# Performance work log

Measured on AMD Instinct MI355X. Metric: run time of the kernel, lower is better.

## Reference

```python
import jax, jax.numpy as jnp
import numpy as np

B = 65536
D = 8          # model dim (hard-wired in source)
H = 2          # num_heads
A = 20         # act_size
L = 5          # tokens per embedding stream


def _attn_layer(x, Wqkv, bqkv, Wo, bo, Wl, bl):
    # x: [B, S, D]
    Bx, S, Dx = x.shape
    hd = Dx // H
    qkv = x @ Wqkv.T + bqkv                      # [B, S, 3D]
    q, k, v = jnp.split(qkv, 3, axis=-1)
    def split_heads(t):
        return t.reshape(Bx, S, H, hd).transpose(0, 2, 1, 3)  # [B,H,S,hd]
    q, k, v = split_heads(q), split_heads(k), split_heads(v)
    scores = jnp.einsum('bhqd,bhkd->bhqk', q, k) * (hd ** -0.5)
    attn = jax.nn.softmax(scores, axis=-1)       # dropout inactive at eval
    o = jnp.einsum('bhqk,bhkd->bhqd', attn, v)
    o = o.transpose(0, 2, 1, 3).reshape(Bx, S, Dx)
    x = x + (o @ Wo.T + bo)                      # residual after attention
    h = jax.nn.relu(x @ Wl.T + bl)               # linear + relu
    return x + h                                 # second residual


def setup_inputs() -> dict:
    key = jax.random.key(0)
    ks = jax.random.split(key, 20)
    s = 1.0 / np.sqrt(D)
    inp = {
        'dice_type': jax.random.randint(ks[0], (B, L), 0, 15),
        'dice_star': jax.random.randint(ks[1], (B, L), 0, 15),
        'summon_lvl': jax.random.randint(ks[2], (B, L), 0, 2),
        'emb_dice': jax.random.normal(ks[3], (15, D), jnp.float32),
        'emb_star': jax.random.normal(ks[4], (15, D), jnp.float32),
        'emb_btns': jax.random.normal(ks[5], (2, D), jnp.float32),
        'Wout': jax.random.normal(ks[6], (A, D), jnp.float32) * s,
        'bout': jnp.zeros((A,), jnp.float32),
    }
    for i in range(2):
        o = 7 + 5 * i
        inp[f'Wqkv{i}'] = jax.random.normal(ks[o], (3 * D, D), jnp.float32) * s
        inp[f'bqkv{i}'] = jnp.zeros((3 * D,), jnp.float32)
        inp[f'Wo{i}'] = jax.random.normal(ks[o + 1], (D, D), jnp.float32) * s
        inp[f'bo{i}'] = jnp.zeros((D,), jnp.float32)
        inp[f'Wl{i}'] = jax.random.normal(ks[o + 2], (D, D), jnp.float32) * s
        inp[f'bl{i}'] = jnp.zeros((D,), jnp.float32)
    return inp


def reference(dice_type, dice_star, summon_lvl,
              emb_dice, emb_star, emb_btns,
              Wqkv0, bqkv0, Wo0, bo0, Wl0, bl0,
              Wqkv1, bqkv1, Wo1, bo1, Wl1, bl1,
              Wout, bout):
    x = jnp.concatenate([emb_dice[dice_type],
                         emb_star[dice_star],
                         emb_btns[summon_lvl]], axis=1)  # [B, 15, D]
    x = _attn_layer(x, Wqkv0, bqkv0, Wo0, bo0, Wl0, bl0)
    x = _attn_layer(x, Wqkv1, bqkv1, Wo1, bo1, Wl1, bl1)
    x = jnp.mean(x, axis=1)                               # [B, D]
    return x @ Wout.T + bout                              # [B, A]
```

## Files before the change

kernel.cpp:

```cpp
#include <hip/hip_runtime.h>
#include <math.h>

#define EPB 16
#define BTOT 65536

__device__ __forceinline__ float fast_exp2(float x) {
#if defined(__has_builtin)
#if __has_builtin(__builtin_amdgcn_exp2f)
  return __builtin_amdgcn_exp2f(x);
#else
  return exp2f(x);
#endif
#else
  return exp2f(x);
#endif
}

__device__ __forceinline__ void attn_layer(
    float x[8], int e, int t,
    const float* __restrict__ Wqkv, const float* __restrict__ bqkv,
    const float* __restrict__ Wo, const float* __restrict__ bo,
    const float* __restrict__ Wl, const float* __restrict__ bl,
    float (*kb)[17][8], float (*vb)[17][8])
{
  float q[8];
  if (t < 15) {
    float k[8], v[8];
#pragma unroll
    for (int c = 0; c < 8; ++c) {
      float aq = bqkv[c];
      float ak = bqkv[8 + c];
      float av = bqkv[16 + c];
#pragma unroll
      for (int j = 0; j < 8; ++j) {
        aq = fmaf(x[j], Wqkv[c * 8 + j], aq);
        ak = fmaf(x[j], Wqkv[(8 + c) * 8 + j], ak);
        av = fmaf(x[j], Wqkv[(16 + c) * 8 + j], av);
      }
      q[c] = aq; k[c] = ak; v[c] = av;
    }
    float4* kd = (float4*)kb[e][t];
    kd[0] = make_float4(k[0], k[1], k[2], k[3]);
    kd[1] = make_float4(k[4], k[5], k[6], k[7]);
    float4* vd = (float4*)vb[e][t];
    vd[0] = make_float4(v[0], v[1], v[2], v[3]);
    vd[1] = make_float4(v[4], v[5], v[6], v[7]);
  }
  __syncthreads();
  if (t < 15) {
    float s0[15], s1[15];
#pragma unroll
    for (int u = 0; u < 15; ++u) {
      const float4 k0 = *(const float4*)(kb[e][u]);
      const float4 k1 = *(const float4*)(kb[e][u] + 4);
      float a0 = q[0] * k0.x;
      a0 = fmaf(q[1], k0.y, a0); a0 = fmaf(q[2], k0.z, a0); a0 = fmaf(q[3], k0.w, a0);
      float a1 = q[4] * k1.x;
      a1 = fmaf(q[5], k1.y, a1); a1 = fmaf(q[6], k1.z, a1); a1 = fmaf(q[7], k1.w, a1);
      s0[u] = a0 * 0.5f;
      s1[u] = a1 * 0.5f;
    }
    float m0 = s0[0], m1 = s1[0];
#pragma unroll
    for (int u = 1; u < 15; ++u) { m0 = fmaxf(m0, s0[u]); m1 = fmaxf(m1, s1[u]); }
    float sum0 = 0.f, sum1 = 0.f;
#pragma unroll
    for (int u = 0; u < 15; ++u) {
      s0[u] = fast_exp2((s0[u] - m0) * 1.4426950408889634f);
      s1[u] = fast_exp2((s1[u] - m1) * 1.4426950408889634f);
      sum0 += s0[u]; sum1 += s1[u];
    }
    const float r0 = 1.0f / sum0, r1 = 1.0f / sum1;
    float o[8] = {0.f, 0.f, 0.f, 0.f, 0.f, 0.f, 0.f, 0.f};
#pragma unroll
    for (int u = 0; u < 15; ++u) {
      const float4 v0 = *(const float4*)(vb[e][u]);
      const float4 v1 = *(const float4*)(vb[e][u] + 4);
      o[0] = fmaf(s0[u], v0.x, o[0]); o[1] = fmaf(s0[u], v0.y, o[1]);
      o[2] = fmaf(s0[u], v0.z, o[2]); o[3] = fmaf(s0[u], v0.w, o[3]);
      o[4] = fmaf(s1[u], v1.x, o[4]); o[5] = fmaf(s1[u], v1.y, o[5]);
      o[6] = fmaf(s1[u], v1.z, o[6]); o[7] = fmaf(s1[u], v1.w, o[7]);
    }
#pragma unroll
    for (int d = 0; d < 4; ++d) { o[d] *= r0; o[4 + d] *= r1; }
    float xn[8];
#pragma unroll
    for (int c = 0; c < 8; ++c) {
      float acc = bo[c];
#pragma unroll
      for (int j = 0; j < 8; ++j) acc = fmaf(o[j], Wo[c * 8 + j], acc);
      xn[c] = x[c] + acc;
    }
#pragma unroll
    for (int c = 0; c < 8; ++c) {
      float acc = bl[c];
#pragma unroll
      for (int j = 0; j < 8; ++j) acc = fmaf(xn[j], Wl[c * 8 + j], acc);
      x[c] = xn[c] + fmaxf(acc, 0.0f);
    }
  }
  __syncthreads();
}

__global__ __launch_bounds__(256) void BetterBot_44169443672375_kernel(
    const int* __restrict__ dice_type, const int* __restrict__ dice_star,
    const int* __restrict__ summon_lvl,
    const float* __restrict__ emb_dice, const float* __restrict__ emb_star,
    const float* __restrict__ emb_btns,
    const float* __restrict__ Wout, const float* __restrict__ bout,
    const float* __restrict__ Wqkv0, const float* __restrict__ bqkv0,
    const float* __restrict__ Wo0, const float* __restrict__ bo0,
    const float* __restrict__ Wl0, const float* __restrict__ bl0,
    const float* __restrict__ Wqkv1, const float* __restrict__ bqkv1,
    const float* __restrict__ Wo1, const float* __restrict__ bo1,
    const float* __restrict__ Wl1, const float* __restrict__ bl1,
    float* __restrict__ out)
{
  __shared__ __align__(16) float kb[EPB][17][8];
  __shared__ __align__(16) float vb[EPB][17][8];
  const int tid = threadIdx.x;
  const int e = tid >> 4;
  const int t = tid & 15;
  const int ge = blockIdx.x * EPB + e;

  float x[8];
  if (t < 15) {
    const float* row;
    if (t < 5)       row = emb_dice + 8 * dice_type[ge * 5 + t];
    else if (t < 10) row = emb_star + 8 * dice_star[ge * 5 + (t - 5)];
    else             row = emb_btns + 8 * summon_lvl[ge * 5 + (t - 10)];
    const float4 r0 = *(const float4*)row;
    const float4 r1 = *(const float4*)(row + 4);
    x[0] = r0.x; x[1] = r0.y; x[2] = r0.z; x[3] = r0.w;
    x[4] = r1.x; x[5] = r1.y; x[6] = r1.z; x[7] = r1.w;
  }

  attn_layer(x, e, t, Wqkv0, bqkv0, Wo0, bo0, Wl0, bl0, kb, vb);
  attn_layer(x, e, t, Wqkv1, bqkv1, Wo1, bo1, Wl1, bl1, kb, vb);

  if (t < 15) {
    float4* xd = (float4*)kb[e][t];
    xd[0] = make_float4(x[0], x[1], x[2], x[3]);
    xd[1] = make_float4(x[4], x[5], x[6], x[7]);
  }
  __syncthreads();
  if (t < 8) {
    float s = 0.f;
#pragma unroll
    for (int u = 0; u < 15; ++u) s += kb[e][u][t];
    vb[e][0][t] = s * (1.0f / 15.0f);
  }
  __syncthreads();
  const int obase = blockIdx.x * (EPB * 20);
  for (int idx = tid; idx < EPB * 20; idx += 256) {
    const int e2 = idx / 20;
    const int a = idx - e2 * 20;
    const float* mr = vb[e2][0];
    float acc = bout[a];
#pragma unroll
    for (int j = 0; j < 8; ++j) acc = fmaf(mr[j], Wout[a * 8 + j], acc);
    out[obase + idx] = acc;
  }
}

extern "C" void kernel_launch(void* const* d_in, const int* in_sizes, int n_in,
                              void* d_out, int out_size, void* d_ws, size_t ws_size,
                              hipStream_t stream) {
  const int*   dice_type  = (const int*)d_in[0];
  const int*   dice_star  = (const int*)d_in[1];
  const int*   summon_lvl = (const int*)d_in[2];
  const float* emb_dice   = (const float*)d_in[3];
  const float* emb_star   = (const float*)d_in[4];
  const float* emb_btns   = (const float*)d_in[5];
  const float* Wout       = (const float*)d_in[6];
  const float* bout       = (const float*)d_in[7];
  const float* Wqkv0      = (const float*)d_in[8];
  const float* bqkv0      = (const float*)d_in[9];
  const float* Wo0        = (const float*)d_in[10];
  const float* bo0        = (const float*)d_in[11];
  const float* Wl0        = (const float*)d_in[12];
  const float* bl0        = (const float*)d_in[13];
  const float* Wqkv1      = (const float*)d_in[14];
  const float* bqkv1      = (const float*)d_in[15];
  const float* Wo1        = (const float*)d_in[16];
  const float* bo1        = (const float*)d_in[17];
  const float* Wl1        = (const float*)d_in[18];
  const float* bl1        = (const float*)d_in[19];
  float* out = (float*)d_out;

  dim3 grid(BTOT / EPB), block(256);
  hipLaunchKernelGGL(BetterBot_44169443672375_kernel, grid, block, 0, stream,
                     dice_type, dice_star, summon_lvl,
                     emb_dice, emb_star, emb_btns, Wout, bout,
                     Wqkv0, bqkv0, Wo0, bo0, Wl0, bl0,
                     Wqkv1, bqkv1, Wo1, bo1, Wl1, bl1,
                     out);
}
```

Measured before the change: 138.8 us.

## Map two tokens per thread, fuse softmax without max, shuffle-reduce mean

Each thread now processes two tokens, so 8 lanes cover one 15-token element and a block handles 32 elements. The separate max, exp and sum passes are fused into a single loop over keys, with the softmax scale and log2(e) folded into q. The max subtraction is dropped. The sequence mean is computed with cross-lane shuffles instead of shared memory and two extra barriers, and each lane writes part of its element's output row directly. This reduces barriers and the passes over K/V in LDS, and spreads the projection and attention work over more lanes. In exchange, register pressure per thread roughly doubles, and skipping the max subtraction risks exp overflow if scores grow large.

```diff
diff --git a/kernel.cpp b/kernel.cpp
--- a/kernel.cpp
+++ b/kernel.cpp
@@ -1,10 +1,12 @@
 #include <hip/hip_runtime.h>
 #include <math.h>
 
-#define EPB 16
+#define EPB 32
+#define ESTRIDE 132
 #define BTOT 65536
-
-__device__ __forceinline__ float fast_exp2(float x) {
+#define C_SCALE 0.72134752044f
+
+__device__ __forceinline__ float exp2_fast(float x) {
 #if defined(__has_builtin)
 #if __has_builtin(__builtin_amdgcn_exp2f)
   return __builtin_amdgcn_exp2f(x);
@@ -17,14 +19,15 @@
 }
 
 __device__ __forceinline__ void attn_layer(
-    float x[8], int e, int t,
+    float x[2][8], float* kb, float* vb, int g,
     const float* __restrict__ Wqkv, const float* __restrict__ bqkv,
     const float* __restrict__ Wo, const float* __restrict__ bo,
-    const float* __restrict__ Wl, const float* __restrict__ bl,
-    float (*kb)[17][8], float (*vb)[17][8])
+    const float* __restrict__ Wl, const float* __restrict__ bl)
 {
-  float q[8];
-  if (t < 15) {
+  float q[2][8];
+#pragma unroll
+  for (int i = 0; i < 2; ++i) {
+    const int t = 2 * g + i;
     float k[8], v[8];
 #pragma unroll
     for (int c = 0; c < 8; ++c) {
@@ -33,70 +36,65 @@
       float av = bqkv[16 + c];
 #pragma unroll
       for (int j = 0; j < 8; ++j) {
-        aq = fmaf(x[j], Wqkv[c * 8 + j], aq);
-        ak = fmaf(x[j], Wqkv[(8 + c) * 8 + j], ak);
-        av = fmaf(x[j], Wqkv[(16 + c) * 8 + j], av);
+        aq = fmaf(x[i][j], Wqkv[c * 8 + j], aq);
+        ak = fmaf(x[i][j], Wqkv[(8 + c) * 8 + j], ak);
+        av = fmaf(x[i][j], Wqkv[(16 + c) * 8 + j], av);
       }
-      q[c] = aq; k[c] = ak; v[c] = av;
-    }
-    float4* kd = (float4*)kb[e][t];
+      q[i][c] = aq * C_SCALE;
+      k[c] = ak; v[c] = av;
+    }
+    float4* kd = (float4*)(kb + t * 8);
     kd[0] = make_float4(k[0], k[1], k[2], k[3]);
     kd[1] = make_float4(k[4], k[5], k[6], k[7]);
-    float4* vd = (float4*)vb[e][t];
+    float4* vd = (float4*)(vb + t * 8);
     vd[0] = make_float4(v[0], v[1], v[2], v[3]);
     vd[1] = make_float4(v[4], v[5], v[6], v[7]);
   }
   __syncthreads();
-  if (t < 15) {
-    float s0[15], s1[15];
-#pragma unroll
-    for (int u = 0; u < 15; ++u) {
-      const float4 k0 = *(const float4*)(kb[e][u]);
-      const float4 k1 = *(const float4*)(kb[e][u] + 4);
-      float a0 = q[0] * k0.x;
-      a0 = fmaf(q[1], k0.y, a0); a0 = fmaf(q[2], k0.z, a0); a0 = fmaf(q[3], k0.w, a0);
-      float a1 = q[4] * k1.x;
-      a1 = fmaf(q[5], k1.y, a1); a1 = fmaf(q[6], k1.z, a1); a1 = fmaf(q[7], k1.w, a1);
-      s0[u] = a0 * 0.5f;
-      s1[u] = a1 * 0.5f;
-    }
-    float m0 = s0[0], m1 = s1[0];
-#pragma unroll
-    for (int u = 1; u < 15; ++u) { m0 = fmaxf(m0, s0[u]); m1 = fmaxf(m1, s1[u]); }
-    float sum0 = 0.f, sum1 = 0.f;
-#pragma unroll
-    for (int u = 0; u < 15; ++u) {
-      s0[u] = fast_exp2((s0[u] - m0) * 1.4426950408889634f);
-      s1[u] = fast_exp2((s1[u] - m1) * 1.4426950408889634f);
-      sum0 += s0[u]; sum1 += s1[u];
-    }
-    const float r0 = 1.0f / sum0, r1 = 1.0f / sum1;
-    float o[8] = {0.f, 0.f, 0.f, 0.f, 0.f, 0.f, 0.f, 0.f};
-#pragma unroll
-    for (int u = 0; u < 15; ++u) {
-      const float4 v0 = *(const float4*)(vb[e][u]);
-      const float4 v1 = *(const float4*)(vb[e][u] + 4);
-      o[0] = fmaf(s0[u], v0.x, o[0]); o[1] = fmaf(s0[u], v0.y, o[1]);
-      o[2] = fmaf(s0[u], v0.z, o[2]); o[3] = fmaf(s0[u], v0.w, o[3]);
-      o[4] = fmaf(s1[u], v1.x, o[4]); o[5] = fmaf(s1[u], v1.y, o[5]);
-      o[6] = fmaf(s1[u], v1.z, o[6]); o[7] = fmaf(s1[u], v1.w, o[7]);
-    }
-#pragma unroll
-    for (int d = 0; d < 4; ++d) { o[d] *= r0; o[4 + d] *= r1; }
+  float o[2][8] = {{0.f,0.f,0.f,0.f,0.f,0.f,0.f,0.f},
+                   {0.f,0.f,0.f,0.f,0.f,0.f,0.f,0.f}};
+  float sum00 = 0.f, sum01 = 0.f, sum10 = 0.f, sum11 = 0.f;
+#pragma unroll
+  for (int u = 0; u < 15; ++u) {
+    const float4 k0 = *(const float4*)(kb + u * 8);
+    const float4 k1 = *(const float4*)(kb + u * 8 + 4);
+    const float4 v0 = *(const float4*)(vb + u * 8);
+    const float4 v1 = *(const float4*)(vb + u * 8 + 4);
+#pragma unroll
+    for (int i = 0; i < 2; ++i) {
+      float s0 = q[i][0] * k0.x;
+      s0 = fmaf(q[i][1], k0.y, s0); s0 = fmaf(q[i][2], k0.z, s0); s0 = fmaf(q[i][3], k0.w, s0);
+      float s1 = q[i][4] * k1.x;
+      s1 = fmaf(q[i][5], k1.y, s1); s1 = fmaf(q[i][6], k1.z, s1); s1 = fmaf(q[i][7], k1.w, s1);
+      const float e0 = exp2_fast(s0);
+      const float e1 = exp2_fast(s1);
+      if (i == 0) { sum00 += e0; sum01 += e1; } else { sum10 += e0; sum11 += e1; }
+      o[i][0] = fmaf(e0, v0.x, o[i][0]); o[i][1] = fmaf(e0, v0.y, o[i][1]);
+      o[i][2] = fmaf(e0, v0.z, o[i][2]); o[i][3] = fmaf(e0, v0.w, o[i][3]);
+      o[i][4] = fmaf(e1, v1.x, o[i][4]); o[i][5] = fmaf(e1, v1.y, o[i][5]);
+      o[i][6] = fmaf(e1, v1.z, o[i][6]); o[i][7] = fmaf(e1, v1.w, o[i][7]);
+    }
+  }
+#pragma unroll
+  for (int i = 0; i < 2; ++i) {
+    const float r0 = 1.0f / (i == 0 ? sum00 : sum10);
+    const float r1 = 1.0f / (i == 0 ? sum01 : sum11);
+#pragma unroll
+    for (int d = 0; d < 4; ++d) { o[i][d] *= r0; o[i][4 + d] *= r1; }
     float xn[8];
 #pragma unroll
     for (int c = 0; c < 8; ++c) {
       float acc = bo[c];
 #pragma unroll
-      for (int j = 0; j < 8; ++j) acc = fmaf(o[j], Wo[c * 8 + j], acc);
-      xn[c] = x[c] + acc;
+      for (int j = 0; j < 8; ++j) acc = fmaf(o[i][j], Wo[c * 8 + j], acc);
+      xn[c] = x[i][c] + acc;
     }
 #pragma unroll
     for (int c = 0; c < 8; ++c) {
       float acc = bl[c];
 #pragma unroll
       for (int j = 0; j < 8; ++j) acc = fmaf(xn[j], Wl[c * 8 + j], acc);
-      x[c] = xn[c] + fmaxf(acc, 0.0f);
+      x[i][c] = xn[c] + fmaxf(acc, 0.0f);
     }
   }
   __syncthreads();
@@ -116,50 +114,61 @@
     const float* __restrict__ Wl1, const float* __restrict__ bl1,
     float* __restrict__ out)
 {
-  __shared__ __align__(16) float kb[EPB][17][8];
-  __shared__ __align__(16) float vb[EPB][17][8];
+  __shared__ __align__(16) float kb_s[EPB * ESTRIDE];
+  __shared__ __align__(16) float vb_s[EPB * ESTRIDE];
   const int tid = threadIdx.x;
-  const int e = tid >> 4;
-  const int t = tid & 15;
+  const int e = tid >> 3;
+  const int g = tid & 7;
   const int ge = blockIdx.x * EPB + e;
-
-  float x[8];
-  if (t < 15) {
-    const float* row;
-    if (t < 5)       row = emb_dice + 8 * dice_type[ge * 5 + t];
-    else if (t < 10) row = emb_star + 8 * dice_star[ge * 5 + (t - 5)];
-    else             row = emb_btns + 8 * summon_lvl[ge * 5 + (t - 10)];
-    const float4 r0 = *(const float4*)row;
-    const float4 r1 = *(const float4*)(row + 4);
-    x[0] = r0.x; x[1] = r0.y; x[2] = r0.z; x[3] = r0.w;
-    x[4] = r1.x; x[5] = r1.y; x[6] = r1.z; x[7] = r1.w;
-  }
-
-  attn_layer(x, e, t, Wqkv0, bqkv0, Wo0, bo0, Wl0, bl0, kb, vb);
-  attn_layer(x, e, t, Wqkv1, bqkv1, Wo1, bo1, Wl1, bl1, kb, vb);
-
-  if (t < 15) {
-    float4* xd = (float4*)kb[e][t];
-    xd[0] = make_float4(x[0], x[1], x[2], x[3]);
-    xd[1] = make_float4(x[4], x[5], x[6], x[7]);
-  }
-  __syncthreads();
-  if (t < 8) {
-    float s = 0.f;
-#pragma unroll
-    for (int u = 0; u < 15; ++u) s += kb[e][u][t];
-    vb[e][0][t] = s * (1.0f / 15.0f);
-  }
-  __syncthreads();
-  const int obase = blockIdx.x * (EPB * 20);
-  for (int idx = tid; idx < EPB * 20; idx += 256) {
-    const int e2 = idx / 20;
-    const int a = idx - e2 * 20;
-    const float* mr = vb[e2][0];
-    float acc = bout[a];
-#pragma unroll
-    for (int j = 0; j < 8; ++j) acc = fmaf(mr[j], Wout[a * 8 + j], acc);
-    out[obase + idx] = acc;
+  float* kb = kb_s + e * ESTRIDE;
+  float* vb = vb_s + e * ESTRIDE;
+
+  float x[2][8];
+#pragma unroll
+  for (int i = 0; i < 2; ++i) {
+    const int t = 2 * g + i;
+    if (t < 15) {
+      const float* row;
+      if (t < 5)       row = emb_dice + 8 * dice_type[ge * 5 + t];
+      else if (t < 10) row = emb_star + 8 * dice_star[ge * 5 + (t - 5)];
+      else             row = emb_btns + 8 * summon_lvl[ge * 5 + (t - 10)];
+      const float4 r0 = ((const float4*)row)[0];
+      const float4 r1 = ((const float4*)row)[1];
+      x[i][0] = r0.x; x[i][1] = r0.y; x[i][2] = r0.z; x[i][3] = r0.w;
+      x[i][4] = r1.x; x[i][5] = r1.y; x[i][6] = r1.z; x[i][7] = r1.w;
+    } else {
+#pragma unroll
+      for (int j = 0; j < 8; ++j) x[i][j] = 0.f;
+    }
+  }
+
+  attn_layer(x, kb, vb, g, Wqkv0, bqkv0, Wo0, bo0, Wl0, bl0);
+  attn_layer(x, kb, vb, g, Wqkv1, bqkv1, Wo1, bo1, Wl1, bl1);
+
+  const bool pad = (g == 7);
+  float p[8];
+#pragma unroll
+  for (int j = 0; j < 8; ++j) p[j] = x[0][j] + (pad ? 0.f : x[1][j]);
+#pragma unroll
+  for (int j = 0; j < 8; ++j) p[j] += __shfl_xor(p[j], 1);
+#pragma unroll
+  for (int j = 0; j < 8; ++j) p[j] += __shfl_xor(p[j], 2);
+#pragma unroll
+  for (int j = 0; j < 8; ++j) p[j] += __shfl_xor(p[j], 4);
+  float mean[8];
+#pragma unroll
+  for (int j = 0; j < 8; ++j) mean[j] = p[j] * (1.0f / 15.0f);
+
+  const int obase = ge * 20;
+#pragma unroll
+  for (int r = 0; r < 3; ++r) {
+    const int a = r * 8 + g;
+    if (a < 20) {
+      float acc = bout[a];
+#pragma unroll
+      for (int j = 0; j < 8; ++j) acc = fmaf(mean[j], Wout[a * 8 + j], acc);
+      out[obase + a] = acc;
+    }
   }
 }
 
```

After: 179.1 us. +29.0%, slower.

## Precompute layer-0 QKV and attention exps over the 32-token vocabulary table

Applied to the files above, without the earlier changes.

Layer 0 depends only on the token index, so each block computes QKV for all 32 possible embedding rows and the full 32x32 table of unnormalised exp scores once. Each token then gathers from these shared tables instead of doing its own projection and dot products. Layer 1 drops the max subtraction and fuses the exp into the PV loop, with the softmax scale folded into q. The mean reduction now uses wave shuffles and the output projection is computed directly per element, which removes two barriers. Omitting the max subtraction risks overflow if scores grow large, and every block redundantly rebuilds the table.

```diff
diff --git a/kernel.cpp b/kernel.cpp
--- a/kernel.cpp
+++ b/kernel.cpp
@@ -3,8 +3,10 @@
 
 #define EPB 16
 #define BTOT 65536
-
-__device__ __forceinline__ float fast_exp2(float x) {
+#define C_SCALE 0.72134752044f
+#define QSTR 28
+
+__device__ __forceinline__ float exp2_fast(float x) {
 #if defined(__has_builtin)
 #if __has_builtin(__builtin_amdgcn_exp2f)
   return __builtin_amdgcn_exp2f(x);
@@ -14,92 +16,6 @@
 #else
   return exp2f(x);
 #endif
-}
-
-__device__ __forceinline__ void attn_layer(
-    float x[8], int e, int t,
-    const float* __restrict__ Wqkv, const float* __restrict__ bqkv,
-    const float* __restrict__ Wo, const float* __restrict__ bo,
-    const float* __restrict__ Wl, const float* __restrict__ bl,
-    float (*kb)[17][8], float (*vb)[17][8])
-{
-  float q[8];
-  if (t < 15) {
-    float k[8], v[8];
-#pragma unroll
-    for (int c = 0; c < 8; ++c) {
-      float aq = bqkv[c];
-      float ak = bqkv[8 + c];
-      float av = bqkv[16 + c];
-#pragma unroll
-      for (int j = 0; j < 8; ++j) {
-        aq = fmaf(x[j], Wqkv[c * 8 + j], aq);
-        ak = fmaf(x[j], Wqkv[(8 + c) * 8 + j], ak);
-        av = fmaf(x[j], Wqkv[(16 + c) * 8 + j], av);
-      }
-      q[c] = aq; k[c] = ak; v[c] = av;
-    }
-    float4* kd = (float4*)kb[e][t];
-    kd[0] = make_float4(k[0], k[1], k[2], k[3]);
-    kd[1] = make_float4(k[4], k[5], k[6], k[7]);
-    float4* vd = (float4*)vb[e][t];
-    vd[0] = make_float4(v[0], v[1], v[2], v[3]);
-    vd[1] = make_float4(v[4], v[5], v[6], v[7]);
-  }
-  __syncthreads();
-  if (t < 15) {
-    float s0[15], s1[15];
-#pragma unroll
-    for (int u = 0; u < 15; ++u) {
-      const float4 k0 = *(const float4*)(kb[e][u]);
-      const float4 k1 = *(const float4*)(kb[e][u] + 4);
-      float a0 = q[0] * k0.x;
-      a0 = fmaf(q[1], k0.y, a0); a0 = fmaf(q[2], k0.z, a0); a0 = fmaf(q[3], k0.w, a0);
-      float a1 = q[4] * k1.x;
-      a1 = fmaf(q[5], k1.y, a1); a1 = fmaf(q[6], k1.z, a1); a1 = fmaf(q[7], k1.w, a1);
-      s0[u] = a0 * 0.5f;
-      s1[u] = a1 * 0.5f;
-    }
-    float m0 = s0[0], m1 = s1[0];
-#pragma unroll
-    for (int u = 1; u < 15; ++u) { m0 = fmaxf(m0, s0[u]); m1 = fmaxf(m1, s1[u]); }
-    float sum0 = 0.f, sum1 = 0.f;
-#pragma unroll
-    for (int u = 0; u < 15; ++u) {
-      s0[u] = fast_exp2((s0[u] - m0) * 1.4426950408889634f);
-      s1[u] = fast_exp2((s1[u] - m1) * 1.4426950408889634f);
-      sum0 += s0[u]; sum1 += s1[u];
-    }
-    const float r0 = 1.0f / sum0, r1 = 1.0f / sum1;
-    float o[8] = {0.f, 0.f, 0.f, 0.f, 0.f, 0.f, 0.f, 0.f};
-#pragma unroll
-    for (int u = 0; u < 15; ++u) {
-      const float4 v0 = *(const float4*)(vb[e][u]);
-      const float4 v1 = *(const float4*)(vb[e][u] + 4);
-      o[0] = fmaf(s0[u], v0.x, o[0]); o[1] = fmaf(s0[u], v0.y, o[1]);
-      o[2] = fmaf(s0[u], v0.z, o[2]); o[3] = fmaf(s0[u], v0.w, o[3]);
-      o[4] = fmaf(s1[u], v1.x, o[4]); o[5] = fmaf(s1[u], v1.y, o[5]);
-      o[6] = fmaf(s1[u], v1.z, o[6]); o[7] = fmaf(s1[u], v1.w, o[7]);
-    }
-#pragma unroll
-    for (int d = 0; d < 4; ++d) { o[d] *= r0; o[4 + d] *= r1; }
-    float xn[8];
-#pragma unroll
-    for (int c = 0; c < 8; ++c) {
-      float acc = bo[c];
-#pragma unroll
-      for (int j = 0; j < 8; ++j) acc = fmaf(o[j], Wo[c * 8 + j], acc);
-      xn[c] = x[c] + acc;
-    }
-#pragma unroll
-    for (int c = 0; c < 8; ++c) {
-      float acc = bl[c];
-#pragma unroll
-      for (int j = 0; j < 8; ++j) acc = fmaf(xn[j], Wl[c * 8 + j], acc);
-      x[c] = xn[c] + fmaxf(acc, 0.0f);
-    }
-  }
-  __syncthreads();
 }
 
 __global__ __launch_bounds__(256) void BetterBot_44169443672375_kernel(
@@ -116,50 +32,204 @@
     const float* __restrict__ Wl1, const float* __restrict__ bl1,
     float* __restrict__ out)
 {
+  __shared__ __align__(16) float qkvT[32 * QSTR];
+  __shared__ __align__(8)  float2 eT[32 * 33];
+  __shared__ __align__(16) float xT[32][8];
+  __shared__ int idxT[EPB][17];
   __shared__ __align__(16) float kb[EPB][17][8];
   __shared__ __align__(16) float vb[EPB][17][8];
+
   const int tid = threadIdx.x;
   const int e = tid >> 4;
   const int t = tid & 15;
   const int ge = blockIdx.x * EPB + e;
 
-  float x[8];
+  int myc = 0;
   if (t < 15) {
-    const float* row;
-    if (t < 5)       row = emb_dice + 8 * dice_type[ge * 5 + t];
-    else if (t < 10) row = emb_star + 8 * dice_star[ge * 5 + (t - 5)];
-    else             row = emb_btns + 8 * summon_lvl[ge * 5 + (t - 10)];
-    const float4 r0 = *(const float4*)row;
-    const float4 r1 = *(const float4*)(row + 4);
-    x[0] = r0.x; x[1] = r0.y; x[2] = r0.z; x[3] = r0.w;
-    x[4] = r1.x; x[5] = r1.y; x[6] = r1.z; x[7] = r1.w;
-  }
-
-  attn_layer(x, e, t, Wqkv0, bqkv0, Wo0, bo0, Wl0, bl0, kb, vb);
-  attn_layer(x, e, t, Wqkv1, bqkv1, Wo1, bo1, Wl1, bl1, kb, vb);
-
+    int c;
+    if (t < 5)       c = dice_type[ge * 5 + t];
+    else if (t < 10) c = 15 + dice_star[ge * 5 + (t - 5)];
+    else             c = 30 + summon_lvl[ge * 5 + (t - 10)];
+    idxT[e][t] = c;
+    myc = c;
+  }
+  {
+    const int c = tid >> 3;
+    const int l8 = tid & 7;
+    const float* er;
+    if (c < 15)      er = emb_dice + 8 * c;
+    else if (c < 30) er = emb_star + 8 * (c - 15);
+    else             er = emb_btns + 8 * (c - 30);
+    const float4 r0 = ((const float4*)er)[0];
+    const float4 r1 = ((const float4*)er)[1];
+    float r[8] = {r0.x, r0.y, r0.z, r0.w, r1.x, r1.y, r1.z, r1.w};
+    xT[c][l8] = r[l8];
+#pragma unroll
+    for (int cc = 0; cc < 3; ++cc) {
+      const int col = l8 * 3 + cc;
+      float acc = bqkv0[col];
+#pragma unroll
+      for (int j = 0; j < 8; ++j) acc = fmaf(r[j], Wqkv0[col * 8 + j], acc);
+      qkvT[c * QSTR + col] = acc;
+    }
+  }
+  __syncthreads();
+
+  {
+    const int p0 = tid * 4;
+    const int qi = p0 >> 5;
+    const float* qr = qkvT + qi * QSTR;
+    float qv[8];
+#pragma unroll
+    for (int j = 0; j < 8; ++j) qv[j] = qr[j];
+#pragma unroll
+    for (int jj = 0; jj < 4; ++jj) {
+      const int ki = (p0 & 31) + jj;
+      const float* kr = qkvT + ki * QSTR + 8;
+      float s0 = qv[0] * kr[0];
+      s0 = fmaf(qv[1], kr[1], s0); s0 = fmaf(qv[2], kr[2], s0); s0 = fmaf(qv[3], kr[3], s0);
+      float s1 = qv[4] * kr[4];
+      s1 = fmaf(qv[5], kr[5], s1); s1 = fmaf(qv[6], kr[6], s1); s1 = fmaf(qv[7], kr[7], s1);
+      eT[qi * 33 + ki] = make_float2(exp2_fast(C_SCALE * s0), exp2_fast(C_SCALE * s1));
+    }
+  }
+  __syncthreads();
+
+  float x[8] = {0.f, 0.f, 0.f, 0.f, 0.f, 0.f, 0.f, 0.f};
+  float q1[8];
   if (t < 15) {
-    float4* xd = (float4*)kb[e][t];
-    xd[0] = make_float4(x[0], x[1], x[2], x[3]);
-    xd[1] = make_float4(x[4], x[5], x[6], x[7]);
+    const float4 x0a = *(const float4*)(xT[myc]);
+    const float4 x0b = *(const float4*)(xT[myc] + 4);
+    x[0] = x0a.x; x[1] = x0a.y; x[2] = x0a.z; x[3] = x0a.w;
+    x[4] = x0b.x; x[5] = x0b.y; x[6] = x0b.z; x[7] = x0b.w;
+
+    float o[8] = {0.f, 0.f, 0.f, 0.f, 0.f, 0.f, 0.f, 0.f};
+    float sum0 = 0.f, sum1 = 0.f;
+    const float2* myE = eT + myc * 33;
+#pragma unroll
+    for (int u = 0; u < 15; ++u) {
+      const int uc = idxT[e][u];
+      const float2 ee = myE[uc];
+      const float4 v0 = *(const float4*)(qkvT + uc * QSTR + 16);
+      const float4 v1 = *(const float4*)(qkvT + uc * QSTR + 20);
+      sum0 += ee.x; sum1 += ee.y;
+      o[0] = fmaf(ee.x, v0.x, o[0]); o[1] = fmaf(ee.x, v0.y, o[1]);
+      o[2] = fmaf(ee.x, v0.z, o[2]); o[3] = fmaf(ee.x, v0.w, o[3]);
+      o[4] = fmaf(ee.y, v1.x, o[4]); o[5] = fmaf(ee.y, v1.y, o[5]);
+      o[6] = fmaf(ee.y, v1.z, o[6]); o[7] = fmaf(ee.y, v1.w, o[7]);
+    }
+    const float r0 = 1.0f / sum0, r1 = 1.0f / sum1;
+#pragma unroll
+    for (int d = 0; d < 4; ++d) { o[d] *= r0; o[4 + d] *= r1; }
+    float xn[8];
+#pragma unroll
+    for (int c = 0; c < 8; ++c) {
+      float acc = bo0[c];
+#pragma unroll
+      for (int j = 0; j < 8; ++j) acc = fmaf(o[j], Wo0[c * 8 + j], acc);
+      xn[c] = x[c] + acc;
+    }
+#pragma unroll
+    for (int c = 0; c < 8; ++c) {
+      float acc = bl0[c];
+#pragma unroll
+      for (int j = 0; j < 8; ++j) acc = fmaf(xn[j], Wl0[c * 8 + j], acc);
+      x[c] = xn[c] + fmaxf(acc, 0.0f);
+    }
+
+    float k1[8], v1[8];
+#pragma unroll
+    for (int c = 0; c < 8; ++c) {
+      float aq = bqkv1[c];
+      float ak = bqkv1[8 + c];
+      float av = bqkv1[16 + c];
+#pragma unroll
+      for (int j = 0; j < 8; ++j) {
+        aq = fmaf(x[j], Wqkv1[c * 8 + j], aq);
+        ak = fmaf(x[j], Wqkv1[(8 + c) * 8 + j], ak);
+        av = fmaf(x[j], Wqkv1[(16 + c) * 8 + j], av);
+      }
+      q1[c] = aq * C_SCALE;
+      k1[c] = ak; v1[c] = av;
+    }
+    float4* kd = (float4*)kb[e][t];
+    kd[0] = make_float4(k1[0], k1[1], k1[2], k1[3]);
+    kd[1] = make_float4(k1[4], k1[5], k1[6], k1[7]);
+    float4* vd = (float4*)vb[e][t];
+    vd[0] = make_float4(v1[0], v1[1], v1[2], v1[3]);
+    vd[1] = make_float4(v1[4], v1[5], v1[6], v1[7]);
   }
   __syncthreads();
-  if (t < 8) {
-    float s = 0.f;
-#pragma unroll
-    for (int u = 0; u < 15; ++u) s += kb[e][u][t];
-    vb[e][0][t] = s * (1.0f / 15.0f);
-  }
-  __syncthreads();
-  const int obase = blockIdx.x * (EPB * 20);
-  for (int idx = tid; idx < EPB * 20; idx += 256) {
-    const int e2 = idx / 20;
-    const int a = idx - e2 * 20;
-    const float* mr = vb[e2][0];
+
+  if (t < 15) {
+    float o[8] = {0.f, 0.f, 0.f, 0.f, 0.f, 0.f, 0.f, 0.f};
+    float sum0 = 0.f, sum1 = 0.f;
+#pragma unroll
+    for (int u = 0; u < 15; ++u) {
+      const float4 k0 = *(const float4*)(kb[e][u]);
+      const float4 k1v = *(const float4*)(kb[e][u] + 4);
+      const float4 v0 = *(const float4*)(vb[e][u]);
+      const float4 v1 = *(const float4*)(vb[e][u] + 4);
+      float s0 = q1[0] * k0.x;
+      s0 = fmaf(q1[1], k0.y, s0); s0 = fmaf(q1[2], k0.z, s0); s0 = fmaf(q1[3], k0.w, s0);
+      float s1 = q1[4] * k1v.x;
+      s1 = fmaf(q1[5], k1v.y, s1); s1 = fmaf(q1[6], k1v.z, s1); s1 = fmaf(q1[7], k1v.w, s1);
+      const float e0 = exp2_fast(s0);
+      const float e1 = exp2_fast(s1);
+      sum0 += e0; sum1 += e1;
+      o[0] = fmaf(e0, v0.x, o[0]); o[1] = fmaf(e0, v0.y, o[1]);
+      o[2] = fmaf(e0, v0.z, o[2]); o[3] = fmaf(e0, v0.w, o[3]);
+      o[4] = fmaf(e1, v1.x, o[4]); o[5] = fmaf(e1, v1.y, o[5]);
+      o[6] = fmaf(e1, v1.z, o[6]); o[7] = fmaf(e1, v1.w, o[7]);
+    }
+    const float r0 = 1.0f / sum0, r1 = 1.0f / sum1;
+#pragma unroll
+    for (int d = 0; d < 4; ++d) { o[d] *= r0; o[4 + d] *= r1; }
+    float xn[8];
+#pragma unroll
+    for (int c = 0; c < 8; ++c) {
+      float acc = bo1[c];
+#pragma unroll
+      for (int j = 0; j < 8; ++j) acc = fmaf(o[j], Wo1[c * 8 + j], acc);
+      xn[c] = x[c] + acc;
+    }
+#pragma unroll
+    for (int c = 0; c < 8; ++c) {
+      float acc = bl1[c];
+#pragma unroll
+      for (int j = 0; j < 8; ++j) acc = fmaf(xn[j], Wl1[c * 8 + j], acc);
+      x[c] = xn[c] + fmaxf(acc, 0.0f);
+    }
+  }
+
+  float p[8];
+#pragma unroll
+  for (int j = 0; j < 8; ++j) p[j] = x[j];
+#pragma unroll
+  for (int j = 0; j < 8; ++j) p[j] += __shfl_xor(p[j], 1);
+#pragma unroll
+  for (int j = 0; j < 8; ++j) p[j] += __shfl_xor(p[j], 2);
+#pragma unroll
+  for (int j = 0; j < 8; ++j) p[j] += __shfl_xor(p[j], 4);
+#pragma unroll
+  for (int j = 0; j < 8; ++j) p[j] += __shfl_xor(p[j], 8);
+  float mean[8];
+#pragma unroll
+  for (int j = 0; j < 8; ++j) mean[j] = p[j] * (1.0f / 15.0f);
+
+  const int obase = ge * 20;
+  {
+    float acc = bout[t];
+#pragma unroll
+    for (int j = 0; j < 8; ++j) acc = fmaf(mean[j], Wout[t * 8 + j], acc);
+    out[obase + t] = acc;
+  }
+  if (t < 4) {
+    const int a = 16 + t;
     float acc = bout[a];
 #pragma unroll
-    for (int j = 0; j < 8; ++j) acc = fmaf(mr[j], Wout[a * 8 + j], acc);
-    out[obase + idx] = acc;
+    for (int j = 0; j < 8; ++j) acc = fmaf(mean[j], Wout[a * 8 + j], acc);
+    out[obase + a] = acc;
   }
 }
 
```

Result: faster. 128.7 us (-7.3%).
